# Kernel optimization log

Measured on AMD Instinct MI355X. Metric: run time of the kernel, lower is better.

The kernel has to match this reference:

```python
import jax, jax.numpy as jnp
import numpy as np

S, B, D, DOUT = 512, 32, 1024, 1024


def setup_inputs() -> dict:
    key = jax.random.key(0)
    ks = jax.random.split(key, 7)
    scale = 1.0 / np.sqrt(D)
    return {
        "x": jax.random.normal(ks[0], (S, B, D), dtype=jnp.float32),
        "w1_w": jax.random.normal(ks[1], (D, D), dtype=jnp.float32) * scale,
        "w1_b": jax.random.normal(ks[2], (D,), dtype=jnp.float32) * scale,
        "w2_w": jax.random.normal(ks[3], (DOUT, D), dtype=jnp.float32) * scale,
        "w2_b": jax.random.normal(ks[4], (DOUT,), dtype=jnp.float32) * scale,
        "model_w": jax.random.normal(ks[5], (DOUT, D), dtype=jnp.float32) * scale,
        "model_b": jax.random.normal(ks[6], (DOUT,), dtype=jnp.float32) * scale,
    }


def reference(x, w1_w, w1_b, w2_w, w2_b, model_w, model_b):
    # x: [S, B, D]; gating vectors from the first token of each sequence
    x0 = x[0]                                   # [B, D]
    v1 = x0 @ w1_w.T + w1_b                     # [B, D]
    v2 = x0 @ w2_w.T + w2_b                     # [B, DOUT]
    # rank-1 outer product gate, sigmoid, elementwise-modulated weight
    mask = jax.nn.sigmoid(v1[:, :, None] * v2[:, None, :])  # [B, D, DOUT]
    mask = mask * model_w.T                     # [B, D, DOUT]
    out = jnp.einsum('sbd,bdf->sbf', x, mask) + model_b      # [S, B, DOUT]
    return out
```

## Files before the change

### kernel.cpp

```cpp
#include <hip/hip_runtime.h>
#include <hip/hip_bf16.h>

#define S_ 512
#define B_ 32
#define D_ 1024
#define F_ 1024
#define XSTRIDE (B_ * D_)

typedef float f32x4 __attribute__((ext_vector_type(4)));
typedef short bf16x8 __attribute__((ext_vector_type(8)));

static __device__ __forceinline__ unsigned short f2bf(float f) {
    __hip_bfloat16 h = __float2bfloat16(f);
    return *reinterpret_cast<unsigned short*>(&h);
}

__global__ __launch_bounds__(256) void vker(
    const float* __restrict__ x,
    const float* __restrict__ w1w, const float* __restrict__ w1b,
    const float* __restrict__ w2w, const float* __restrict__ w2b,
    float* __restrict__ vbuf)
{
    __shared__ float xs[B_][132];
    __shared__ float wst[64][132];
    int fb = blockIdx.x & 31;
    int ks = blockIdx.x >> 5;
    int k0 = ks * 128;
    int t  = threadIdx.x;
    const float* w = (fb < 16) ? w1w : w2w;
    int fbase = (fb < 16) ? fb * 64 : (fb - 16) * 64;

    #pragma unroll
    for (int i = 0; i < 4; ++i) {
        int q = t + 256 * i;
        int row = q >> 5, c4 = (q & 31) * 4;
        float4 v = *reinterpret_cast<const float4*>(x + (size_t)row * D_ + k0 + c4);
        *reinterpret_cast<float4*>(&xs[row][c4]) = v;
    }
    #pragma unroll
    for (int i = 0; i < 8; ++i) {
        int q = t + 256 * i;
        int row = q >> 5, c4 = (q & 31) * 4;
        float4 v = *reinterpret_cast<const float4*>(w + (size_t)(fbase + row) * D_ + k0 + c4);
        *reinterpret_cast<float4*>(&wst[row][c4]) = v;
    }
    __syncthreads();

    int b   = t >> 3;
    int fl0 = t & 7;
    float acc[8] = {0,0,0,0,0,0,0,0};
    for (int k4 = 0; k4 < 32; ++k4) {
        float4 xv = *reinterpret_cast<const float4*>(&xs[b][k4 * 4]);
        #pragma unroll
        for (int j = 0; j < 8; ++j) {
            float4 wv = *reinterpret_cast<const float4*>(&wst[fl0 + 8 * j][k4 * 4]);
            acc[j] += xv.x * wv.x + xv.y * wv.y + xv.z * wv.z + xv.w * wv.w;
        }
    }
    #pragma unroll
    for (int j = 0; j < 8; ++j) {
        int fg = fb * 64 + fl0 + 8 * j;
        float v = acc[j];
        if (ks == 0) v += (fg < 1024) ? w1b[fg] : w2b[fg - 1024];
        if (fg < 1024) v *= -1.44269504088896f;
        atomicAdd(&vbuf[b * 2048 + fg], v);
    }
}

__global__ __launch_bounds__(512) void fused(
    const float* __restrict__ x, const float* __restrict__ mw,
    const float* __restrict__ mb, const float* __restrict__ vbuf,
    float* __restrict__ out)
{
    __shared__ __align__(16) unsigned short As[256 * 64];
    __shared__ __align__(16) unsigned short Bs[128 * 64];
    __shared__ float v2s[128];

    const int bid = blockIdx.x;
    const int b   = (bid & 7) + ((bid >> 3) & 3) * 8;
    const int rem = bid >> 5;
    const int f0  = (rem & 7) * 128;
    const int s0  = (rem >> 3) * 256;

    const int tid  = threadIdx.x;
    const int lane = tid & 63, wid = tid >> 6;
    const int wr = (wid >> 1) * 64;
    const int wc = (wid & 1) * 64;

    if (tid < 128) v2s[tid] = vbuf[b * 2048 + 1024 + f0 + tid];

    const int rbase = tid >> 3;
    const int c8    = tid & 7;
    const int wchunk = ((c8 ^ (rbase & 7)) << 3);

    const float* apt = x  + (size_t)(s0 + rbase) * XSTRIDE + (size_t)b * D_ + c8 * 8;
    const float* wpt = mw + (size_t)(f0 + rbase) * D_ + c8 * 8;
    const float* vpt = vbuf + b * 2048 + c8 * 8;

    unsigned short* Awr = As + rbase * 64 + wchunk;
    unsigned short* Bwr = Bs + rbase * 64 + wchunk;

    f32x4 acc[4][4] = {};
    float4 a[4][2], w[2][2], vv[2];

#define LOADS(K0) do { \
    _Pragma("unroll") for (int p = 0; p < 4; ++p) { \
        a[p][0] = *reinterpret_cast<const float4*>(apt + (size_t)p * (64 * XSTRIDE) + (K0)); \
        a[p][1] = *reinterpret_cast<const float4*>(apt + (size_t)p * (64 * XSTRIDE) + (K0) + 4); } \
    _Pragma("unroll") for (int p = 0; p < 2; ++p) { \
        w[p][0] = *reinterpret_cast<const float4*>(wpt + p * (64 * D_) + (K0)); \
        w[p][1] = *reinterpret_cast<const float4*>(wpt + p * (64 * D_) + (K0) + 4); } \
    vv[0] = *reinterpret_cast<const float4*>(vpt + (K0)); \
    vv[1] = *reinterpret_cast<const float4*>(vpt + (K0) + 4); \
} while (0)

    LOADS(0);
    __syncthreads();
    const float v2r0 = v2s[rbase];
    const float v2r1 = v2s[rbase + 64];

    for (int kt = 0; kt < 16; ++kt) {
        #pragma unroll
        for (int p = 0; p < 4; ++p) {
            union { unsigned short u[8]; bf16x8 v; } pk;
            pk.u[0] = f2bf(a[p][0].x); pk.u[1] = f2bf(a[p][0].y);
            pk.u[2] = f2bf(a[p][0].z); pk.u[3] = f2bf(a[p][0].w);
            pk.u[4] = f2bf(a[p][1].x); pk.u[5] = f2bf(a[p][1].y);
            pk.u[6] = f2bf(a[p][1].z); pk.u[7] = f2bf(a[p][1].w);
            *reinterpret_cast<bf16x8*>(Awr + p * 4096) = pk.v;
        }
        #pragma unroll
        for (int p = 0; p < 2; ++p) {
            const float v2 = p ? v2r1 : v2r0;
            union { unsigned short u[8]; bf16x8 v; } pk;
            pk.u[0] = f2bf(w[p][0].x * __builtin_amdgcn_rcpf(1.0f + __builtin_amdgcn_exp2f(vv[0].x * v2)));
            pk.u[1] = f2bf(w[p][0].y * __builtin_amdgcn_rcpf(1.0f + __builtin_amdgcn_exp2f(vv[0].y * v2)));
            pk.u[2] = f2bf(w[p][0].z * __builtin_amdgcn_rcpf(1.0f + __builtin_amdgcn_exp2f(vv[0].z * v2)));
            pk.u[3] = f2bf(w[p][0].w * __builtin_amdgcn_rcpf(1.0f + __builtin_amdgcn_exp2f(vv[0].w * v2)));
            pk.u[4] = f2bf(w[p][1].x * __builtin_amdgcn_rcpf(1.0f + __builtin_amdgcn_exp2f(vv[1].x * v2)));
            pk.u[5] = f2bf(w[p][1].y * __builtin_amdgcn_rcpf(1.0f + __builtin_amdgcn_exp2f(vv[1].y * v2)));
            pk.u[6] = f2bf(w[p][1].z * __builtin_amdgcn_rcpf(1.0f + __builtin_amdgcn_exp2f(vv[1].z * v2)));
            pk.u[7] = f2bf(w[p][1].w * __builtin_amdgcn_rcpf(1.0f + __builtin_amdgcn_exp2f(vv[1].w * v2)));
            *reinterpret_cast<bf16x8*>(Bwr + p * 4096) = pk.v;
        }
        if (kt < 15) LOADS((kt + 1) * 64);
        asm volatile("s_waitcnt lgkmcnt(0)" ::: "memory");
        __builtin_amdgcn_s_barrier();
        #pragma unroll
        for (int kh = 0; kh < 2; ++kh) {
            const int kslot = (lane >> 4) + kh * 4;
            bf16x8 af[4], bq[4];
            #pragma unroll
            for (int m2 = 0; m2 < 4; ++m2) {
                int r = wr + m2 * 16 + (lane & 15);
                af[m2] = *reinterpret_cast<const bf16x8*>(
                    As + r * 64 + ((kslot ^ (r & 7)) << 3));
            }
            #pragma unroll
            for (int n2 = 0; n2 < 4; ++n2) {
                int r = wc + n2 * 16 + (lane & 15);
                bq[n2] = *reinterpret_cast<const bf16x8*>(
                    Bs + r * 64 + ((kslot ^ (r & 7)) << 3));
            }
            #pragma unroll
            for (int m2 = 0; m2 < 4; ++m2)
                #pragma unroll
                for (int n2 = 0; n2 < 4; ++n2)
                    acc[m2][n2] = __builtin_amdgcn_mfma_f32_16x16x32_bf16(
                        af[m2], bq[n2], acc[m2][n2], 0, 0, 0);
        }
        __builtin_amdgcn_s_barrier();
    }
#undef LOADS

    const int col = lane & 15, rg = (lane >> 4) * 4;
    float bias[4];
    #pragma unroll
    for (int n2 = 0; n2 < 4; ++n2) bias[n2] = mb[f0 + wc + n2 * 16 + col];
    #pragma unroll
    for (int m2 = 0; m2 < 4; ++m2)
        #pragma unroll
        for (int n2 = 0; n2 < 4; ++n2)
            #pragma unroll
            for (int r = 0; r < 4; ++r) {
                int srow = s0 + wr + m2 * 16 + rg + r;
                out[(size_t)srow * (B_ * F_) + b * F_ + f0 + wc + n2 * 16 + col]
                    = acc[m2][n2][r] + bias[n2];
            }
}

extern "C" void kernel_launch(void* const* d_in, const int* in_sizes, int n_in,
                              void* d_out, int out_size, void* d_ws, size_t ws_size,
                              hipStream_t stream) {
    const float* x   = (const float*)d_in[0];
    const float* w1w = (const float*)d_in[1];
    const float* w1b = (const float*)d_in[2];
    const float* w2w = (const float*)d_in[3];
    const float* w2b = (const float*)d_in[4];
    const float* mw  = (const float*)d_in[5];
    const float* mb  = (const float*)d_in[6];
    float* outp = (float*)d_out;
    float* vbuf = (float*)d_ws;

    hipMemsetAsync(vbuf, 0, B_ * 2048 * sizeof(float), stream);
    vker<<<256, 256, 0, stream>>>(x, w1w, w1b, w2w, w2b, vbuf);
    fused<<<512, 512, 0, stream>>>(x, mw, mb, vbuf, outp);
}
```

Baseline: 213.9 us.

## Pre-convert x and model weights to bf16 and stream A tiles via global_load_lds

Adds two conversion kernels. One turns x into a bf16 buffer laid out batch-major and pre-swizzled for the LDS tile pattern; the other turns model_w into bf16. The main GEMM kernel then loads A tiles straight from global memory into LDS with global_load_lds, and reads the bf16 weights, using v_cvt_pk_bf16_f32 for packing. This removes the per-tile fp32-to-bf16 conversion and register staging of x, and halves the bytes of the repeated x reads across f-blocks. In exchange it adds an extra full pass over x (read fp32, write bf16) plus two kernel launches.

Measured after the change: 201.4 us. 5.8% less time.

```diff
diff --git a/kernel.cpp b/kernel.cpp
--- a/kernel.cpp
+++ b/kernel.cpp
@@ -5,14 +5,15 @@
 #define B_ 32
 #define D_ 1024
 #define F_ 1024
-#define XSTRIDE (B_ * D_)
 
 typedef float f32x4 __attribute__((ext_vector_type(4)));
 typedef short bf16x8 __attribute__((ext_vector_type(8)));
-
-static __device__ __forceinline__ unsigned short f2bf(float f) {
-    __hip_bfloat16 h = __float2bfloat16(f);
-    return *reinterpret_cast<unsigned short*>(&h);
+typedef unsigned u32x4 __attribute__((ext_vector_type(4)));
+
+static __device__ __forceinline__ unsigned cvtpk(float lo, float hi) {
+    unsigned r;
+    asm("v_cvt_pk_bf16_f32 %0, %1, %2" : "=v"(r) : "v"(lo), "v"(hi));
+    return r;
 }
 
 __global__ __launch_bounds__(256) void vker(
@@ -67,8 +68,37 @@
     }
 }
 
-__global__ __launch_bounds__(512) void fused(
-    const float* __restrict__ x, const float* __restrict__ mw,
+__global__ __launch_bounds__(256) void xcvt(
+    const float* __restrict__ x, unsigned short* __restrict__ xb)
+{
+    int g = blockIdx.x * 256 + threadIdx.x;
+    int c  = g & 7;
+    int kt = (g >> 3) & 15;
+    int s  = (g >> 7) & 511;
+    int b  = g >> 16;
+    const float* src = x + (((size_t)(s * B_ + b)) << 10) + kt * 64 + ((c ^ (s & 7)) << 3);
+    float4 a0 = *reinterpret_cast<const float4*>(src);
+    float4 a1 = *reinterpret_cast<const float4*>(src + 4);
+    u32x4 pk = { cvtpk(a0.x, a0.y), cvtpk(a0.z, a0.w),
+                 cvtpk(a1.x, a1.y), cvtpk(a1.z, a1.w) };
+    *reinterpret_cast<u32x4*>(xb + ((size_t)g << 3)) = pk;
+}
+
+__global__ __launch_bounds__(256) void mwcvt(
+    const float* __restrict__ mw, unsigned short* __restrict__ mwb)
+{
+    int g = blockIdx.x * 256 + threadIdx.x;
+    const float* src = mw + ((size_t)g << 3);
+    float4 a0 = *reinterpret_cast<const float4*>(src);
+    float4 a1 = *reinterpret_cast<const float4*>(src + 4);
+    u32x4 pk = { cvtpk(a0.x, a0.y), cvtpk(a0.z, a0.w),
+                 cvtpk(a1.x, a1.y), cvtpk(a1.z, a1.w) };
+    *reinterpret_cast<u32x4*>(mwb + ((size_t)g << 3)) = pk;
+}
+
+__global__ __launch_bounds__(512) void fused2(
+    const unsigned short* __restrict__ xb,
+    const unsigned short* __restrict__ mwb,
     const float* __restrict__ mb, const float* __restrict__ vbuf,
     float* __restrict__ out)
 {
@@ -89,62 +119,66 @@
 
     if (tid < 128) v2s[tid] = vbuf[b * 2048 + 1024 + f0 + tid];
 
+    const unsigned short* adma = xb
+        + ((size_t)(b * S_ + s0 + wid * 8 + (lane >> 3))) * D_ + ((lane & 7) << 3);
+    unsigned short* alds = As + (wid * 8) * 64;
+
     const int rbase = tid >> 3;
     const int c8    = tid & 7;
-    const int wchunk = ((c8 ^ (rbase & 7)) << 3);
-
-    const float* apt = x  + (size_t)(s0 + rbase) * XSTRIDE + (size_t)b * D_ + c8 * 8;
-    const float* wpt = mw + (size_t)(f0 + rbase) * D_ + c8 * 8;
-    const float* vpt = vbuf + b * 2048 + c8 * 8;
-
-    unsigned short* Awr = As + rbase * 64 + wchunk;
-    unsigned short* Bwr = Bs + rbase * 64 + wchunk;
+    const unsigned short* wpt = mwb + (size_t)(f0 + rbase) * D_ + (c8 << 3);
+    const float* vpt = vbuf + b * 2048 + (c8 << 3);
+    unsigned short* Bwr = Bs + rbase * 64 + ((c8 ^ (rbase & 7)) << 3);
 
     f32x4 acc[4][4] = {};
-    float4 a[4][2], w[2][2], vv[2];
-
-#define LOADS(K0) do { \
-    _Pragma("unroll") for (int p = 0; p < 4; ++p) { \
-        a[p][0] = *reinterpret_cast<const float4*>(apt + (size_t)p * (64 * XSTRIDE) + (K0)); \
-        a[p][1] = *reinterpret_cast<const float4*>(apt + (size_t)p * (64 * XSTRIDE) + (K0) + 4); } \
-    _Pragma("unroll") for (int p = 0; p < 2; ++p) { \
-        w[p][0] = *reinterpret_cast<const float4*>(wpt + p * (64 * D_) + (K0)); \
-        w[p][1] = *reinterpret_cast<const float4*>(wpt + p * (64 * D_) + (K0) + 4); } \
-    vv[0] = *reinterpret_cast<const float4*>(vpt + (K0)); \
-    vv[1] = *reinterpret_cast<const float4*>(vpt + (K0) + 4); \
-} while (0)
-
-    LOADS(0);
+    bf16x8 mwv0, mwv1;
+    float4 vva, vvb;
+
+    mwv0 = *reinterpret_cast<const bf16x8*>(wpt);
+    mwv1 = *reinterpret_cast<const bf16x8*>(wpt + 64 * D_);
+    vva  = *reinterpret_cast<const float4*>(vpt);
+    vvb  = *reinterpret_cast<const float4*>(vpt + 4);
     __syncthreads();
     const float v2r0 = v2s[rbase];
     const float v2r1 = v2s[rbase + 64];
 
     for (int kt = 0; kt < 16; ++kt) {
-        #pragma unroll
-        for (int p = 0; p < 4; ++p) {
-            union { unsigned short u[8]; bf16x8 v; } pk;
-            pk.u[0] = f2bf(a[p][0].x); pk.u[1] = f2bf(a[p][0].y);
-            pk.u[2] = f2bf(a[p][0].z); pk.u[3] = f2bf(a[p][0].w);
-            pk.u[4] = f2bf(a[p][1].x); pk.u[5] = f2bf(a[p][1].y);
-            pk.u[6] = f2bf(a[p][1].z); pk.u[7] = f2bf(a[p][1].w);
-            *reinterpret_cast<bf16x8*>(Awr + p * 4096) = pk.v;
-        }
-        #pragma unroll
-        for (int p = 0; p < 2; ++p) {
-            const float v2 = p ? v2r1 : v2r0;
-            union { unsigned short u[8]; bf16x8 v; } pk;
-            pk.u[0] = f2bf(w[p][0].x * __builtin_amdgcn_rcpf(1.0f + __builtin_amdgcn_exp2f(vv[0].x * v2)));
-            pk.u[1] = f2bf(w[p][0].y * __builtin_amdgcn_rcpf(1.0f + __builtin_amdgcn_exp2f(vv[0].y * v2)));
-            pk.u[2] = f2bf(w[p][0].z * __builtin_amdgcn_rcpf(1.0f + __builtin_amdgcn_exp2f(vv[0].z * v2)));
-            pk.u[3] = f2bf(w[p][0].w * __builtin_amdgcn_rcpf(1.0f + __builtin_amdgcn_exp2f(vv[0].w * v2)));
-            pk.u[4] = f2bf(w[p][1].x * __builtin_amdgcn_rcpf(1.0f + __builtin_amdgcn_exp2f(vv[1].x * v2)));
-            pk.u[5] = f2bf(w[p][1].y * __builtin_amdgcn_rcpf(1.0f + __builtin_amdgcn_exp2f(vv[1].y * v2)));
-            pk.u[6] = f2bf(w[p][1].z * __builtin_amdgcn_rcpf(1.0f + __builtin_amdgcn_exp2f(vv[1].z * v2)));
-            pk.u[7] = f2bf(w[p][1].w * __builtin_amdgcn_rcpf(1.0f + __builtin_amdgcn_exp2f(vv[1].w * v2)));
-            *reinterpret_cast<bf16x8*>(Bwr + p * 4096) = pk.v;
-        }
-        if (kt < 15) LOADS((kt + 1) * 64);
-        asm volatile("s_waitcnt lgkmcnt(0)" ::: "memory");
+        const int k0 = kt * 64;
+        #pragma unroll
+        for (int p = 0; p < 4; ++p)
+            __builtin_amdgcn_global_load_lds(
+                (const __attribute__((address_space(1))) void*)(adma + (size_t)p * (64 * D_) + k0),
+                (__attribute__((address_space(3))) void*)(alds + p * 4096),
+                16, 0, 0);
+        __builtin_amdgcn_sched_barrier(0);
+        {
+            union { bf16x8 v; unsigned short u[8]; } m0, m1;
+            m0.v = mwv0; m1.v = mwv1;
+            float vf[8] = { vva.x, vva.y, vva.z, vva.w, vvb.x, vvb.y, vvb.z, vvb.w };
+            float p0[8], p1[8];
+            #pragma unroll
+            for (int j = 0; j < 8; ++j) {
+                float w0 = __uint_as_float((unsigned)(unsigned short)m0.u[j] << 16);
+                float w1 = __uint_as_float((unsigned)(unsigned short)m1.u[j] << 16);
+                float e0 = __builtin_amdgcn_exp2f(vf[j] * v2r0);
+                float e1 = __builtin_amdgcn_exp2f(vf[j] * v2r1);
+                p0[j] = w0 * __builtin_amdgcn_rcpf(1.0f + e0);
+                p1[j] = w1 * __builtin_amdgcn_rcpf(1.0f + e1);
+            }
+            u32x4 o0 = { cvtpk(p0[0], p0[1]), cvtpk(p0[2], p0[3]),
+                         cvtpk(p0[4], p0[5]), cvtpk(p0[6], p0[7]) };
+            u32x4 o1 = { cvtpk(p1[0], p1[1]), cvtpk(p1[2], p1[3]),
+                         cvtpk(p1[4], p1[5]), cvtpk(p1[6], p1[7]) };
+            *reinterpret_cast<u32x4*>(Bwr) = o0;
+            *reinterpret_cast<u32x4*>(Bwr + 64 * 64) = o1;
+        }
+        {
+            const int k1 = ((kt + 1) & 15) * 64;
+            mwv0 = *reinterpret_cast<const bf16x8*>(wpt + k1);
+            mwv1 = *reinterpret_cast<const bf16x8*>(wpt + 64 * D_ + k1);
+            vva  = *reinterpret_cast<const float4*>(vpt + k1);
+            vvb  = *reinterpret_cast<const float4*>(vpt + k1 + 4);
+        }
+        asm volatile("s_waitcnt vmcnt(4) lgkmcnt(0)" ::: "memory");
         __builtin_amdgcn_s_barrier();
         #pragma unroll
         for (int kh = 0; kh < 2; ++kh) {
@@ -171,7 +205,6 @@
         }
         __builtin_amdgcn_s_barrier();
     }
-#undef LOADS
 
     const int col = lane & 15, rg = (lane >> 4) * 4;
     float bias[4];
@@ -200,9 +233,14 @@
     const float* mw  = (const float*)d_in[5];
     const float* mb  = (const float*)d_in[6];
     float* outp = (float*)d_out;
+
     float* vbuf = (float*)d_ws;
+    unsigned short* xbp  = (unsigned short*)((char*)d_ws + ((size_t)1 << 20));
+    unsigned short* mwbp = (unsigned short*)((char*)d_ws + ((size_t)35 << 20));
 
     hipMemsetAsync(vbuf, 0, B_ * 2048 * sizeof(float), stream);
     vker<<<256, 256, 0, stream>>>(x, w1w, w1b, w2w, w2b, vbuf);
-    fused<<<512, 512, 0, stream>>>(x, mw, mb, vbuf, outp);
-}
+    xcvt<<<8192, 256, 0, stream>>>(x, xbp);
+    mwcvt<<<512, 256, 0, stream>>>(mw, mwbp);
+    fused2<<<512, 512, 0, stream>>>(xbp, mwbp, mb, vbuf, outp);
+}
```
